# Optimization experiments

Measured on AMD Instinct MI355X. Metric: run time of the kernel, lower is better.

Reference implementation:

```python
import jax, jax.numpy as jnp
import numpy as np

N = 50000
E = 800000
T = 5            # towers
F = 10           # in_num / F_in per tower (divide_input=False)
F_OUT = 2        # out_channels // towers
G = 64           # number of graphs in the batch
L = 2            # conv layers
BN_EPS = 1e-5
STD_EPS = 1e-5


def setup_inputs() -> dict:
    key = jax.random.key(0)
    ks = jax.random.split(key, 24)
    s = 0.1
    inp = {
        'x': jax.random.normal(ks[0], (N, F), jnp.float32),
        'edge_emb': jax.random.normal(ks[1], (4, F), jnp.float32) * s,
        'mlp1_w1': jax.random.normal(ks[2], (F, 5), jnp.float32) * s,
        'mlp1_b1': jnp.zeros((5,), jnp.float32),
        'mlp1_w2': jax.random.normal(ks[3], (5, F), jnp.float32) * s,
        'mlp1_b2': jnp.zeros((F,), jnp.float32),
        'enc_w': jax.random.normal(ks[4], (L, F, F), jnp.float32) * s,
        'enc_b': jnp.zeros((L, F), jnp.float32),
        'pre_w': jax.random.normal(ks[5], (L, T, 3 * F, F), jnp.float32) * s,
        'pre_b': jnp.zeros((L, T, F), jnp.float32),
        'post_w': jax.random.normal(ks[6], (L, T, 13 * F, F_OUT), jnp.float32) * s,
        'post_b': jnp.zeros((L, T, F_OUT), jnp.float32),
        'lin_w': jax.random.normal(ks[7], (L, F, F), jnp.float32) * s,
        'lin_b': jnp.zeros((L, F), jnp.float32),
        'bn_gamma': jnp.ones((L, F), jnp.float32),
        'bn_beta': jnp.zeros((L, F), jnp.float32),
        'mlp2_w1': jax.random.normal(ks[8], (F, 5), jnp.float32) * s,
        'mlp2_b1': jnp.zeros((5,), jnp.float32),
        'mlp2_w2': jax.random.normal(ks[9], (5, 1), jnp.float32) * s,
        'mlp2_b2': jnp.zeros((1,), jnp.float32),
        'edge_index': jax.random.randint(ks[10], (2, E), 0, N, jnp.int64),
        'edge_attr': jax.random.randint(ks[11], (E,), 0, 4, jnp.int64),
        'batch': jnp.sort(jax.random.randint(ks[12], (N,), 0, G, jnp.int64)),
    }
    return inp


def reference(x, edge_emb, mlp1_w1, mlp1_b1, mlp1_w2, mlp1_b2,
              enc_w, enc_b, pre_w, pre_b, post_w, post_b, lin_w, lin_b,
              bn_gamma, bn_beta, mlp2_w1, mlp2_b1, mlp2_w2, mlp2_b2,
              edge_index, edge_attr, batch):
    src, dst = edge_index[0], edge_index[1]
    # mlp1: 10 -> 5 -> 10
    h = jax.nn.relu(x @ mlp1_w1 + mlp1_b1) @ mlp1_w2 + mlp1_b2  # [N, F]
    ea = edge_emb[edge_attr]  # [E, F] edge embedding lookup

    # in-degree at target nodes, PNA degree statistics
    deg = jax.ops.segment_sum(jnp.ones((src.shape[0],), h.dtype), dst, num_segments=N)
    d = jnp.clip(deg, 1.0)
    avg_log = jnp.mean(jnp.log(deg + 1.0))  # avg_deg['log'] from degree distribution
    log_d = jnp.log(d + 1.0)
    amp = (log_d / avg_log)[:, None, None]
    att = (avg_log / log_d)[:, None, None]
    has_in = (deg > 0)[:, None, None]
    inv_d = (1.0 / d)[:, None, None]

    for l in range(L):
        e = ea @ enc_w[l] + enc_b[l]  # [E, F]
        # message = pre_nn(cat(x_i, x_j, edge_attr)) per tower (x shared across towers)
        msg_in = jnp.concatenate([h[dst], h[src], e], axis=-1)  # [E, 3F]
        m = jnp.einsum('ef,tfo->eto', msg_in, pre_w[l]) + pre_b[l]  # [E, T, F]
        mean = jax.ops.segment_sum(m, dst, num_segments=N) * inv_d
        mean2 = jax.ops.segment_sum(m * m, dst, num_segments=N) * inv_d
        std = jnp.sqrt(jax.nn.relu(mean2 - mean * mean) + STD_EPS)
        mn = jnp.where(has_in, jax.ops.segment_min(m, dst, num_segments=N), 0.0)
        mx = jnp.where(has_in, jax.ops.segment_max(m, dst, num_segments=N), 0.0)
        agg = jnp.concatenate([mean, mn, mx, std], axis=-1)  # [N, T, 4F]
        agg = jnp.concatenate([agg, agg * amp, agg * att], axis=-1)  # [N, T, 12F]
        xt = jnp.broadcast_to(h[:, None, :], (h.shape[0], T, F))
        o = jnp.concatenate([xt, agg], axis=-1)  # [N, T, 13F]
        o = jnp.einsum('ntf,tfo->nto', o, post_w[l]) + post_b[l]  # [N, T, F_OUT]
        o = o.reshape(o.shape[0], T * F_OUT) @ lin_w[l] + lin_b[l]  # [N, F]
        # train-mode BatchNorm over nodes
        mu = jnp.mean(o, axis=0)
        var = jnp.var(o, axis=0)
        o = (o - mu) / jnp.sqrt(var + BN_EPS) * bn_gamma[l] + bn_beta[l]
        h = jax.nn.relu(o)

    g = jax.ops.segment_sum(h, batch, num_segments=G)  # global_add_pool -> [G, F]
    out = jax.nn.relu(g @ mlp2_w1 + mlp2_b1) @ mlp2_w2 + mlp2_b2  # [G, 1]
    return out
```

## Files before the change

### kernel.cpp

```cpp
#include <hip/hip_runtime.h>
#include <math.h>

#define N_NODES 50000
#define N_EDGES 800000
#define G_GRAPHS 64
#define BSTRIDE 64
#define CPAD 16

#define WAVE_SYNC() asm volatile("s_waitcnt lgkmcnt(0)" ::: "memory")
#define RFL(v) __builtin_amdgcn_readfirstlane(v)

__global__ void k_mlp1(const float* __restrict__ x,
                       const float* __restrict__ w1, const float* __restrict__ b1,
                       const float* __restrict__ w2, const float* __restrict__ b2,
                       float* __restrict__ h,
                       int* __restrict__ cnt,
                       float* __restrict__ bn_part, float* __restrict__ g,
                       float* __restrict__ avg_log,
                       const float* __restrict__ edge_emb,
                       const float* __restrict__ enc_w, const float* __restrict__ enc_b,
                       const float* __restrict__ pre_w, float* __restrict__ encm,
                       float* __restrict__ u) {
  __shared__ float eo[2][4][10];
  __shared__ float sw[500];
  int tid = threadIdx.x;
  int n = blockIdx.x * blockDim.x + tid;
  if (n < 1280) bn_part[n] = 0.f;
  if (n < G_GRAPHS * 10) g[n] = 0.f;
  if (n == 0) avg_log[0] = 0.f;

  bool act = n < N_NODES;
  float hr[10];
  if (act) {
    cnt[n * CPAD] = 0;
    float xv[10];
#pragma unroll
    for (int k = 0; k < 10; k++) xv[k] = x[n * 10 + k];
    float hid[5];
#pragma unroll
    for (int j = 0; j < 5; j++) {
      float a = b1[j];
#pragma unroll
      for (int k = 0; k < 10; k++) a += xv[k] * w1[k * 5 + j];
      hid[j] = fmaxf(a, 0.f);
    }
#pragma unroll
    for (int f = 0; f < 10; f++) {
      float a = b2[f];
#pragma unroll
      for (int j = 0; j < 5; j++) a += hid[j] * w2[j * 10 + f];
      hr[f] = a;
      h[n * 10 + f] = a;
    }
  }
  for (int j = tid; j < 500; j += 256) {
    int t = j / 100, k = (j / 10) % 10, f = j % 10;
    sw[j] = pre_w[(t * 30 + 10 + k) * 10 + f];
  }
  if (blockIdx.x == 0) {
    for (int i = tid; i < 80; i += 256) {
      int l = i / 40; int a = (i / 10) % 4; int k = i % 10;
      float s = enc_b[l * 10 + k];
      for (int j = 0; j < 10; j++) s += edge_emb[a * 10 + j] * enc_w[(l * 10 + j) * 10 + k];
      eo[l][a][k] = s;
    }
  }
  __syncthreads();
  if (blockIdx.x == 0) {
    for (int i = tid; i < 400; i += 256) {
      int l = i / 200; int a = (i / 50) % 4; int t = (i / 10) % 5; int f = i % 10;
      float s = 0.f;
      for (int k = 0; k < 10; k++) s += eo[l][a][k] * pre_w[((l * 5 + t) * 30 + 20 + k) * 10 + f];
      encm[i] = s;
    }
  }
  if (act) {
    float2* up = (float2*)(u + n * 50);
#pragma unroll
    for (int c0 = 0; c0 < 25; c0++) {
      int ca = 2 * c0, cb = 2 * c0 + 1;
      int ta = ca / 10, fa = ca % 10, tb = cb / 10, fb = cb % 10;
      float a = 0.f, b = 0.f;
#pragma unroll
      for (int k = 0; k < 10; k++) {
        a += hr[k] * sw[ta * 100 + fa + k * 10];
        b += hr[k] * sw[tb * 100 + fb + k * 10];
      }
      up[c0] = make_float2(a, b);
    }
  }
}

__global__ void k_scatter(const int* __restrict__ src, const int* __restrict__ dst,
                          const int* __restrict__ attr,
                          int* __restrict__ cnt, int* __restrict__ epk) {
  int e = blockIdx.x * blockDim.x + threadIdx.x;
  if (e >= N_EDGES) return;
  int d = dst[e];
  int s = src[e];
  int a = attr[e];
  int k = atomicAdd(&cnt[d * CPAD], 1);
  if (k < BSTRIDE) epk[d * BSTRIDE + k] = s * 200 + a;
}

__global__ void k_avg(const int* __restrict__ cnt, float* __restrict__ avg_log) {
  __shared__ float ws[4];
  int tid = threadIdx.x;
  float acc = 0.f;
  for (int n = blockIdx.x * 256 + tid; n < N_NODES; n += gridDim.x * 256)
    acc += __logf((float)cnt[n * CPAD] + 1.f);
#pragma unroll
  for (int d = 32; d >= 1; d >>= 1) acc += __shfl_down(acc, d, 64);
  if ((tid & 63) == 0) ws[tid >> 6] = acc;
  __syncthreads();
  if (tid == 0) atomicAdd(avg_log, ws[0] + ws[1] + ws[2] + ws[3]);
}

__global__ __launch_bounds__(256) void k_conv(
    const float* __restrict__ h,
    const float* __restrict__ u,
    const float* __restrict__ pre_w_l,
    const float* __restrict__ pre_b_l,
    const float* __restrict__ post_w_l,
    const float* __restrict__ post_b_l,
    const float* __restrict__ lin_w_l,
    const float* __restrict__ lin_b_l,
    const float* __restrict__ encm_l,
    const int* __restrict__ cnt,
    const int* __restrict__ epk,
    const float* __restrict__ avg_log_p,
    float* __restrict__ o_buf,
    float* __restrict__ bn_part)
{
  __shared__ float sW[1300];
  __shared__ float sLin[100];
  __shared__ float sLb[10];
  __shared__ float sPb[10];
  __shared__ float sP[4][100];
  __shared__ float sO[4][10];
  __shared__ float bnS[10], bnQ[10];

  int tid = threadIdx.x;
  int wid = RFL(tid >> 6);
  int lane = tid & 63;
  for (int i = tid; i < 1300; i += 256) sW[i] = post_w_l[i];
  for (int i = tid; i < 100; i += 256) sLin[i] = lin_w_l[i];
  if (tid < 10) {
    sLb[tid] = lin_b_l[tid];
    sPb[tid] = post_b_l[tid];
    bnS[tid] = 0.f; bnQ[tid] = 0.f;
  }
  __syncthreads();

  int f = lane % 10;
  int t = (lane < 50) ? (lane / 10) : 4;
  int c50 = t * 10 + f;
  const char* ub = (const char*)u;
  int c50_4 = c50 * 4;
  float wdst[10];
#pragma unroll
  for (int k = 0; k < 10; k++) wdst[k] = pre_w_l[(t * 30 + k) * 10 + f];
  float em0 = encm_l[c50];
  float em1 = encm_l[50 + c50];
  float em2 = encm_l[100 + c50];
  float em3 = encm_l[150 + c50];
  float preb = pre_b_l[c50];
  float avg_log = avg_log_p[0] * (1.f / N_NODES);

  int n = blockIdx.x * 4 + wid;
  float bnSv = 0.f, bnQv = 0.f;

#define PRE(US, AS, IDX) { int sp_ = __builtin_amdgcn_readlane(pk, (IDX) & 63); \
    AS = sp_ & 3; US = 0.f; \
    if ((IDX) < deg) US = *(const float*)(ub + (sp_ & ~7) + c50_4); }
#define PROC(US, AS) { float m_ = ((AS & 2) ? ((AS & 1) ? bem3 : bem2) : ((AS & 1) ? bem1 : bem0)) + US; \
    sum += m_; sq = fmaf(m_, m_, sq); mnv = fminf(mnv, m_); mxv = fmaxf(mxv, m_); }

  if (n < N_NODES) {
    int deg = cnt[n * CPAD];
    if (deg > BSTRIDE) deg = BSTRIDE;
    int pk = (lane < deg) ? epk[n * BSTRIDE + lane] : 0;

    const float* hn = h + n * 10;
    float2 d0 = *(const float2*)hn;
    float2 d1 = *(const float2*)(hn + 2);
    float2 d2 = *(const float2*)(hn + 4);
    float2 d3 = *(const float2*)(hn + 6);
    float2 d4 = *(const float2*)(hn + 8);
    float xf = hn[f];

    float base = preb
      + d0.x * wdst[0] + d0.y * wdst[1] + d1.x * wdst[2] + d1.y * wdst[3]
      + d2.x * wdst[4] + d2.y * wdst[5] + d3.x * wdst[6] + d3.y * wdst[7]
      + d4.x * wdst[8] + d4.y * wdst[9];
    float bem0 = base + em0, bem1 = base + em1, bem2 = base + em2, bem3 = base + em3;

    float sum = 0.f, sq = 0.f, mnv = INFINITY, mxv = -INFINITY;
    {
      float u0, u1, u2, u3, u4, u5, u6, u7;
      int a0, a1, a2, a3, a4, a5, a6, a7;
      PRE(u0, a0, 0) PRE(u1, a1, 1) PRE(u2, a2, 2) PRE(u3, a3, 3)
      PRE(u4, a4, 4) PRE(u5, a5, 5) PRE(u6, a6, 6) PRE(u7, a7, 7)
      int full = deg & ~7;
      int jb = 0;
      for (; jb < full; jb += 8) {
        PROC(u0, a0) PRE(u0, a0, jb + 8)
        PROC(u1, a1) PRE(u1, a1, jb + 9)
        PROC(u2, a2) PRE(u2, a2, jb + 10)
        PROC(u3, a3) PRE(u3, a3, jb + 11)
        PROC(u4, a4) PRE(u4, a4, jb + 12)
        PROC(u5, a5) PRE(u5, a5, jb + 13)
        PROC(u6, a6) PRE(u6, a6, jb + 14)
        PROC(u7, a7) PRE(u7, a7, jb + 15)
      }
      if (jb + 0 < deg) PROC(u0, a0)
      if (jb + 1 < deg) PROC(u1, a1)
      if (jb + 2 < deg) PROC(u2, a2)
      if (jb + 3 < deg) PROC(u3, a3)
      if (jb + 4 < deg) PROC(u4, a4)
      if (jb + 5 < deg) PROC(u5, a5)
      if (jb + 6 < deg) PROC(u6, a6)
    }

    float degf = (float)deg;
    float d = fmaxf(degf, 1.f);
    float inv = 1.f / d;
    float mean = sum * inv;
    float var = sq * inv - mean * mean;
    float stdv = sqrtf(fmaxf(var, 0.f) + 1e-5f);
    if (deg == 0) { mnv = 0.f; mxv = 0.f; }
    float log_d = logf(d + 1.f);
    float amp = log_d / avg_log;
    float att = avg_log / log_d;

    float vv[13];
    vv[0] = xf;
    vv[1] = mean;       vv[2] = mnv;        vv[3] = mxv;        vv[4] = stdv;
    vv[5] = mean * amp; vv[6] = mnv * amp;  vv[7] = mxv * amp;  vv[8] = stdv * amp;
    vv[9] = mean * att; vv[10] = mnv * att; vv[11] = mxv * att; vv[12] = stdv * att;
    float p0 = 0.f, p1 = 0.f;
#pragma unroll
    for (int j = 0; j < 13; j++) {
      const float2 w = *(const float2*)&sW[t * 260 + (f + 10 * j) * 2];
      p0 += vv[j] * w.x; p1 += vv[j] * w.y;
    }
    if (lane < 50) *(float2*)&sP[wid][c50 * 2] = make_float2(p0, p1);
    WAVE_SYNC();
    if (lane < 10) {
      int tt = lane >> 1, c = lane & 1;
      float o = sPb[lane];
#pragma unroll
      for (int ff = 0; ff < 10; ff++) o += sP[wid][(tt * 10 + ff) * 2 + c];
      sO[wid][lane] = o;
    }
    WAVE_SYNC();
    if (lane < 10) {
      float r = sLb[lane];
#pragma unroll
      for (int j = 0; j < 10; j++) r += sO[wid][j] * sLin[j * 10 + lane];
      o_buf[n * 10 + lane] = r;
      bnSv = r; bnQv = r * r;
    }
  }
#undef PRE
#undef PROC

  if (lane < 10) {
    atomicAdd(&bnS[lane], bnSv);
    atomicAdd(&bnQ[lane], bnQv);
  }
  __syncthreads();
  if (tid < 20) {
    float v = (tid < 10) ? bnS[tid] : bnQ[tid - 10];
    atomicAdd(&bn_part[(blockIdx.x & 31) * 20 + tid], v);
  }
}

__global__ __launch_bounds__(256) void k_bnpool(
    const float* __restrict__ o_buf,
    const float* __restrict__ bn_part,
    const float* __restrict__ gamma, const float* __restrict__ beta,
    float* __restrict__ h,
    const int* __restrict__ batch, float* __restrict__ g,
    const float* __restrict__ pre_w_next, float* __restrict__ u,
    int do_u, int do_pool) {
  __shared__ float sS[20];
  __shared__ float sMu[10], sInv[10];
  __shared__ float pool[8][10];
  __shared__ float hrow[25][10];
  __shared__ float sw[500];
  __shared__ int g0s;
  int tid = threadIdx.x;
  int n0 = blockIdx.x * 25;
  if (do_u) {
    for (int j = tid; j < 500; j += 256) {
      int t = j / 100, k = (j / 10) % 10, f = j % 10;
      sw[j] = pre_w_next[(t * 30 + 10 + k) * 10 + f];
    }
  }
  if (tid < 20) {
    float s = 0.f;
    for (int j = 0; j < 32; j++) s += bn_part[j * 20 + tid];
    sS[tid] = s;
  }
  if (tid < 80) pool[tid / 10][tid % 10] = 0.f;
  if (tid == 0) g0s = batch[n0];
  __syncthreads();
  if (tid < 10) {
    float mu = sS[tid] * (1.f / N_NODES);
    float var = sS[10 + tid] * (1.f / N_NODES) - mu * mu;
    sMu[tid] = mu;
    sInv[tid] = 1.f / sqrtf(fmaxf(var, 0.f) + 1e-5f);
  }
  __syncthreads();
  if (tid < 250) {
    int dn = tid / 10, f = tid % 10;
    int n = n0 + dn;
    int i = n * 10 + f;
    float o = (o_buf[i] - sMu[f]) * sInv[f] * gamma[f] + beta[f];
    float r = fmaxf(o, 0.f);
    h[i] = r;
    hrow[dn][f] = r;
    if (do_pool) {
      int dg = batch[n] - g0s;
      if (dg < 8) atomicAdd(&pool[dg][f], r);
      else atomicAdd(&g[(g0s + dg) * 10 + f], r);
    }
  }
  __syncthreads();
  if (do_u && tid < 250) {
#pragma unroll
    for (int it = 0; it < 5; it++) {
      int j = tid + it * 250;
      int node = j / 50, c = j % 50;
      int t = c / 10, f2 = c % 10;
      float acc = 0.f;
#pragma unroll
      for (int k = 0; k < 10; k++) acc += hrow[node][k] * sw[t * 100 + f2 + k * 10];
      u[n0 * 50 + j] = acc;
    }
  }
  if (do_pool) {
    __syncthreads();
    if (tid < 80) {
      float v = pool[tid / 10][tid % 10];
      if (v != 0.f) atomicAdd(&g[(g0s + tid / 10) * 10 + tid % 10], v);
    }
  }
}

__global__ void k_mlp2(const float* __restrict__ g,
                       const float* __restrict__ w1, const float* __restrict__ b1,
                       const float* __restrict__ w2, const float* __restrict__ b2,
                       float* __restrict__ out) {
  int b = threadIdx.x;
  if (b >= G_GRAPHS) return;
  float gv[10];
#pragma unroll
  for (int k = 0; k < 10; k++) gv[k] = g[b * 10 + k];
  float acc = b2[0];
#pragma unroll
  for (int j = 0; j < 5; j++) {
    float a = b1[j];
#pragma unroll
    for (int k = 0; k < 10; k++) a += gv[k] * w1[k * 5 + j];
    acc += fmaxf(a, 0.f) * w2[j];
  }
  out[b] = acc;
}

extern "C" void kernel_launch(void* const* d_in, const int* in_sizes, int n_in,
                              void* d_out, int out_size, void* d_ws, size_t ws_size,
                              hipStream_t stream) {
  const float* x        = (const float*)d_in[0];
  const float* edge_emb = (const float*)d_in[1];
  const float* m1w1 = (const float*)d_in[2];
  const float* m1b1 = (const float*)d_in[3];
  const float* m1w2 = (const float*)d_in[4];
  const float* m1b2 = (const float*)d_in[5];
  const float* enc_w = (const float*)d_in[6];
  const float* enc_b = (const float*)d_in[7];
  const float* pre_w = (const float*)d_in[8];
  const float* pre_b = (const float*)d_in[9];
  const float* post_w = (const float*)d_in[10];
  const float* post_b = (const float*)d_in[11];
  const float* lin_w = (const float*)d_in[12];
  const float* lin_b = (const float*)d_in[13];
  const float* bn_g = (const float*)d_in[14];
  const float* bn_b = (const float*)d_in[15];
  const float* m2w1 = (const float*)d_in[16];
  const float* m2b1 = (const float*)d_in[17];
  const float* m2w2 = (const float*)d_in[18];
  const float* m2b2 = (const float*)d_in[19];
  const int* edge_index = (const int*)d_in[20];
  const int* edge_attr  = (const int*)d_in[21];
  const int* batch      = (const int*)d_in[22];
  const int* src  = edge_index;
  const int* dstp = edge_index + N_EDGES;

  char* ws = (char*)d_ws;
  size_t off = 0;
  auto alloc = [&](size_t bytes) {
    void* p = ws + off;
    off += (bytes + 255) & ~(size_t)255;
    return p;
  };
  float*     h       = (float*)alloc(N_NODES * 10 * sizeof(float));
  float*     o_buf   = (float*)alloc(N_NODES * 10 * sizeof(float));
  float*     u       = (float*)alloc((size_t)(N_NODES * 50 + 64) * sizeof(float));
  int*       cnt     = (int*)alloc((size_t)N_NODES * CPAD * sizeof(int));
  int*       epk     = (int*)alloc((size_t)N_NODES * BSTRIDE * sizeof(int));
  float*     encm    = (float*)alloc(400 * sizeof(float));
  float*     avg_log = (float*)alloc(16);
  float*     bn_part = (float*)alloc(2 * 32 * 20 * sizeof(float));
  float*     g       = (float*)alloc(G_GRAPHS * 10 * sizeof(float));

  k_mlp1<<<(N_NODES + 255) / 256, 256, 0, stream>>>(x, m1w1, m1b1, m1w2, m1b2, h,
                                                    cnt, bn_part, g, avg_log,
                                                    edge_emb, enc_w, enc_b, pre_w, encm, u);
  k_scatter<<<(N_EDGES + 255) / 256, 256, 0, stream>>>(src, dstp, edge_attr, cnt, epk);
  k_avg<<<64, 256, 0, stream>>>(cnt, avg_log);

  for (int l = 0; l < 2; l++) {
    k_conv<<<(N_NODES + 3) / 4, 256, 0, stream>>>(
        h, u, pre_w + l * 1500, pre_b + l * 50, post_w + l * 1300, post_b + l * 10,
        lin_w + l * 100, lin_b + l * 10, encm + l * 200,
        cnt, epk, avg_log, o_buf, bn_part + l * 640);
    k_bnpool<<<N_NODES / 25, 256, 0, stream>>>(
        o_buf, bn_part + l * 640, bn_g + l * 10, bn_b + l * 10, h, batch, g,
        pre_w + 1500, u, l == 0, l == 1);
  }
  k_mlp2<<<1, 64, 0, stream>>>(g, m2w1, m2b1, m2w2, m2b2, (float*)d_out);
}
```

Measured before the change: 293.1 us.

## Drop precomputed u projection; gather raw h and project per edge in conv

Removes the per-node precomputed source projection buffer u (50 floats per node) and instead gathers the 10-float h row of each source node, applying the pre-transform weights per edge with cross-lane readlane dot products. It also fuses the mlp1 and edge-scatter kernels into one edge-sized front kernel with a separate counter-zero kernel, and pads the edge lists with sentinel entries pointing to a zeroed h row so the gather needs no bounds check. This cuts gather traffic and removes the u writes in mlp1 and bnpool, at the cost of about 10 extra readlane+FMA steps per edge in the conv kernel.

Result: slower. 348.7 us (+19.0%).

```diff
diff --git a/kernel.cpp b/kernel.cpp
--- a/kernel.cpp
+++ b/kernel.cpp
@@ -6,36 +6,49 @@
 #define G_GRAPHS 64
 #define BSTRIDE 64
 #define CPAD 16
+#define SENPK (N_NODES * 40)
 
 #define WAVE_SYNC() asm volatile("s_waitcnt lgkmcnt(0)" ::: "memory")
 #define RFL(v) __builtin_amdgcn_readfirstlane(v)
-
-__global__ void k_mlp1(const float* __restrict__ x,
-                       const float* __restrict__ w1, const float* __restrict__ b1,
-                       const float* __restrict__ w2, const float* __restrict__ b2,
-                       float* __restrict__ h,
-                       int* __restrict__ cnt,
-                       float* __restrict__ bn_part, float* __restrict__ g,
-                       float* __restrict__ avg_log,
-                       const float* __restrict__ edge_emb,
-                       const float* __restrict__ enc_w, const float* __restrict__ enc_b,
-                       const float* __restrict__ pre_w, float* __restrict__ encm,
-                       float* __restrict__ u) {
+#define RLF(v, k) __int_as_float(__builtin_amdgcn_readlane(__float_as_int(v), (k)))
+
+__global__ void k_zero(int* __restrict__ cnt) {
+  int n = blockIdx.x * 256 + threadIdx.x;
+  if (n < N_NODES) cnt[n * CPAD] = 0;
+}
+
+__global__ __launch_bounds__(256) void k_front(
+    const float* __restrict__ x,
+    const float* __restrict__ w1, const float* __restrict__ b1,
+    const float* __restrict__ w2, const float* __restrict__ b2,
+    float* __restrict__ h,
+    int* __restrict__ cnt,
+    float* __restrict__ bn_part, float* __restrict__ g,
+    float* __restrict__ avg_log,
+    const float* __restrict__ edge_emb,
+    const float* __restrict__ enc_w, const float* __restrict__ enc_b,
+    const float* __restrict__ pre_w, float* __restrict__ encm,
+    const int* __restrict__ src, const int* __restrict__ dst,
+    const int* __restrict__ attr, int* __restrict__ epk) {
   __shared__ float eo[2][4][10];
-  __shared__ float sw[500];
   int tid = threadIdx.x;
-  int n = blockIdx.x * blockDim.x + tid;
-  if (n < 1280) bn_part[n] = 0.f;
-  if (n < G_GRAPHS * 10) g[n] = 0.f;
-  if (n == 0) avg_log[0] = 0.f;
-
-  bool act = n < N_NODES;
-  float hr[10];
-  if (act) {
-    cnt[n * CPAD] = 0;
+  int gid = blockIdx.x * 256 + tid;
+
+  int ed = dst[gid];
+  int es = src[gid];
+  int ea = attr[gid];
+  int rk = atomicAdd(&cnt[ed * CPAD], 1);
+
+  if (gid < 1280) bn_part[gid] = 0.f;
+  if (gid < G_GRAPHS * 10) g[gid] = 0.f;
+  if (gid == 0) avg_log[0] = 0.f;
+  { int z = gid - N_NODES; if (z >= 0 && z < 16) h[N_NODES * 10 + z] = 0.f; }
+
+  if (gid < N_NODES) {
+    const float2* xp = (const float2*)(x + gid * 10);
     float xv[10];
 #pragma unroll
-    for (int k = 0; k < 10; k++) xv[k] = x[n * 10 + k];
+    for (int k = 0; k < 5; k++) { float2 v = xp[k]; xv[2 * k] = v.x; xv[2 * k + 1] = v.y; }
     float hid[5];
 #pragma unroll
     for (int j = 0; j < 5; j++) {
@@ -49,14 +62,12 @@
       float a = b2[f];
 #pragma unroll
       for (int j = 0; j < 5; j++) a += hid[j] * w2[j * 10 + f];
-      hr[f] = a;
-      h[n * 10 + f] = a;
-    }
-  }
-  for (int j = tid; j < 500; j += 256) {
-    int t = j / 100, k = (j / 10) % 10, f = j % 10;
-    sw[j] = pre_w[(t * 30 + 10 + k) * 10 + f];
-  }
+      h[gid * 10 + f] = a;
+    }
+  }
+
+  if (rk < BSTRIDE) epk[ed * BSTRIDE + rk] = es * 40 + ea;
+
   if (blockIdx.x == 0) {
     for (int i = tid; i < 80; i += 256) {
       int l = i / 40; int a = (i / 10) % 4; int k = i % 10;
@@ -74,41 +85,20 @@
       encm[i] = s;
     }
   }
-  if (act) {
-    float2* up = (float2*)(u + n * 50);
-#pragma unroll
-    for (int c0 = 0; c0 < 25; c0++) {
-      int ca = 2 * c0, cb = 2 * c0 + 1;
-      int ta = ca / 10, fa = ca % 10, tb = cb / 10, fb = cb % 10;
-      float a = 0.f, b = 0.f;
-#pragma unroll
-      for (int k = 0; k < 10; k++) {
-        a += hr[k] * sw[ta * 100 + fa + k * 10];
-        b += hr[k] * sw[tb * 100 + fb + k * 10];
-      }
-      up[c0] = make_float2(a, b);
-    }
-  }
-}
-
-__global__ void k_scatter(const int* __restrict__ src, const int* __restrict__ dst,
-                          const int* __restrict__ attr,
-                          int* __restrict__ cnt, int* __restrict__ epk) {
-  int e = blockIdx.x * blockDim.x + threadIdx.x;
-  if (e >= N_EDGES) return;
-  int d = dst[e];
-  int s = src[e];
-  int a = attr[e];
-  int k = atomicAdd(&cnt[d * CPAD], 1);
-  if (k < BSTRIDE) epk[d * BSTRIDE + k] = s * 200 + a;
-}
-
-__global__ void k_avg(const int* __restrict__ cnt, float* __restrict__ avg_log) {
+}
+
+__global__ void k_avg(const int* __restrict__ cnt, float* __restrict__ avg_log,
+                      int* __restrict__ epk) {
   __shared__ float ws[4];
   int tid = threadIdx.x;
   float acc = 0.f;
-  for (int n = blockIdx.x * 256 + tid; n < N_NODES; n += gridDim.x * 256)
-    acc += __logf((float)cnt[n * CPAD] + 1.f);
+  for (int n = blockIdx.x * 256 + tid; n < N_NODES; n += gridDim.x * 256) {
+    int dg = cnt[n * CPAD];
+    acc += __logf((float)dg + 1.f);
+    int dd = dg < BSTRIDE ? dg : BSTRIDE;
+    int end = dd + 8 < BSTRIDE ? dd + 8 : BSTRIDE;
+    for (int j = dd; j < end; j++) epk[n * BSTRIDE + j] = SENPK;
+  }
 #pragma unroll
   for (int d = 32; d >= 1; d >>= 1) acc += __shfl_down(acc, d, 64);
   if ((tid & 63) == 0) ws[tid >> 6] = acc;
@@ -118,7 +108,6 @@
 
 __global__ __launch_bounds__(256) void k_conv(
     const float* __restrict__ h,
-    const float* __restrict__ u,
     const float* __restrict__ pre_w_l,
     const float* __restrict__ pre_b_l,
     const float* __restrict__ post_w_l,
@@ -155,11 +144,13 @@
   int f = lane % 10;
   int t = (lane < 50) ? (lane / 10) : 4;
   int c50 = t * 10 + f;
-  const char* ub = (const char*)u;
-  int c50_4 = c50 * 4;
-  float wdst[10];
+  const char* hb = (const char*)h;
+  int f4 = f * 4;
+  float wdst[10], wsrc[10];
 #pragma unroll
   for (int k = 0; k < 10; k++) wdst[k] = pre_w_l[(t * 30 + k) * 10 + f];
+#pragma unroll
+  for (int k = 0; k < 10; k++) wsrc[k] = pre_w_l[(t * 30 + 10 + k) * 10 + f];
   float em0 = encm_l[c50];
   float em1 = encm_l[50 + c50];
   float em2 = encm_l[100 + c50];
@@ -170,16 +161,19 @@
   int n = blockIdx.x * 4 + wid;
   float bnSv = 0.f, bnQv = 0.f;
 
-#define PRE(US, AS, IDX) { int sp_ = __builtin_amdgcn_readlane(pk, (IDX) & 63); \
-    AS = sp_ & 3; US = 0.f; \
-    if ((IDX) < deg) US = *(const float*)(ub + (sp_ & ~7) + c50_4); }
-#define PROC(US, AS) { float m_ = ((AS & 2) ? ((AS & 1) ? bem3 : bem2) : ((AS & 1) ? bem1 : bem0)) + US; \
+#define PRE(HV, AS, IDX) { int sp_ = __builtin_amdgcn_readlane(pk, (IDX) & 63); \
+    AS = sp_ & 3; \
+    HV = *(const float*)(hb + (sp_ & ~7) + f4); }
+#define PROC(HV, AS) { float us_ = 0.f; \
+    _Pragma("unroll") \
+    for (int k_ = 0; k_ < 10; k_++) us_ += RLF(HV, k_) * wsrc[k_]; \
+    float m_ = ((AS & 2) ? ((AS & 1) ? bem3 : bem2) : ((AS & 1) ? bem1 : bem0)) + us_; \
     sum += m_; sq = fmaf(m_, m_, sq); mnv = fminf(mnv, m_); mxv = fmaxf(mxv, m_); }
 
   if (n < N_NODES) {
-    int deg = cnt[n * CPAD];
+    int deg = RFL(cnt[n * CPAD]);
     if (deg > BSTRIDE) deg = BSTRIDE;
-    int pk = (lane < deg) ? epk[n * BSTRIDE + lane] : 0;
+    int pk = epk[n * BSTRIDE + lane];
 
     const float* hn = h + n * 10;
     float2 d0 = *(const float2*)hn;
@@ -282,22 +276,13 @@
     const float* __restrict__ gamma, const float* __restrict__ beta,
     float* __restrict__ h,
     const int* __restrict__ batch, float* __restrict__ g,
-    const float* __restrict__ pre_w_next, float* __restrict__ u,
-    int do_u, int do_pool) {
+    int do_pool) {
   __shared__ float sS[20];
   __shared__ float sMu[10], sInv[10];
   __shared__ float pool[8][10];
-  __shared__ float hrow[25][10];
-  __shared__ float sw[500];
   __shared__ int g0s;
   int tid = threadIdx.x;
   int n0 = blockIdx.x * 25;
-  if (do_u) {
-    for (int j = tid; j < 500; j += 256) {
-      int t = j / 100, k = (j / 10) % 10, f = j % 10;
-      sw[j] = pre_w_next[(t * 30 + 10 + k) * 10 + f];
-    }
-  }
   if (tid < 20) {
     float s = 0.f;
     for (int j = 0; j < 32; j++) s += bn_part[j * 20 + tid];
@@ -320,24 +305,10 @@
     float o = (o_buf[i] - sMu[f]) * sInv[f] * gamma[f] + beta[f];
     float r = fmaxf(o, 0.f);
     h[i] = r;
-    hrow[dn][f] = r;
     if (do_pool) {
       int dg = batch[n] - g0s;
       if (dg < 8) atomicAdd(&pool[dg][f], r);
       else atomicAdd(&g[(g0s + dg) * 10 + f], r);
-    }
-  }
-  __syncthreads();
-  if (do_u && tid < 250) {
-#pragma unroll
-    for (int it = 0; it < 5; it++) {
-      int j = tid + it * 250;
-      int node = j / 50, c = j % 50;
-      int t = c / 10, f2 = c % 10;
-      float acc = 0.f;
-#pragma unroll
-      for (int k = 0; k < 10; k++) acc += hrow[node][k] * sw[t * 100 + f2 + k * 10];
-      u[n0 * 50 + j] = acc;
     }
   }
   if (do_pool) {
@@ -405,9 +376,8 @@
     off += (bytes + 255) & ~(size_t)255;
     return p;
   };
-  float*     h       = (float*)alloc(N_NODES * 10 * sizeof(float));
+  float*     h       = (float*)alloc((N_NODES * 10 + 16) * sizeof(float));
   float*     o_buf   = (float*)alloc(N_NODES * 10 * sizeof(float));
-  float*     u       = (float*)alloc((size_t)(N_NODES * 50 + 64) * sizeof(float));
   int*       cnt     = (int*)alloc((size_t)N_NODES * CPAD * sizeof(int));
   int*       epk     = (int*)alloc((size_t)N_NODES * BSTRIDE * sizeof(int));
   float*     encm    = (float*)alloc(400 * sizeof(float));
@@ -415,20 +385,22 @@
   float*     bn_part = (float*)alloc(2 * 32 * 20 * sizeof(float));
   float*     g       = (float*)alloc(G_GRAPHS * 10 * sizeof(float));
 
-  k_mlp1<<<(N_NODES + 255) / 256, 256, 0, stream>>>(x, m1w1, m1b1, m1w2, m1b2, h,
-                                                    cnt, bn_part, g, avg_log,
-                                                    edge_emb, enc_w, enc_b, pre_w, encm, u);
-  k_scatter<<<(N_EDGES + 255) / 256, 256, 0, stream>>>(src, dstp, edge_attr, cnt, epk);
-  k_avg<<<64, 256, 0, stream>>>(cnt, avg_log);
+  k_zero<<<(N_NODES + 255) / 256, 256, 0, stream>>>(cnt);
+
+  k_front<<<N_EDGES / 256, 256, 0, stream>>>(x, m1w1, m1b1, m1w2, m1b2, h,
+                                             cnt, bn_part, g, avg_log,
+                                             edge_emb, enc_w, enc_b, pre_w, encm,
+                                             src, dstp, edge_attr, epk);
+  k_avg<<<64, 256, 0, stream>>>(cnt, avg_log, epk);
 
   for (int l = 0; l < 2; l++) {
-    k_conv<<<(N_NODES + 3) / 4, 256, 0, stream>>>(
-        h, u, pre_w + l * 1500, pre_b + l * 50, post_w + l * 1300, post_b + l * 10,
+    k_conv<<<N_NODES / 4, 256, 0, stream>>>(
+        h, pre_w + l * 1500, pre_b + l * 50, post_w + l * 1300, post_b + l * 10,
         lin_w + l * 100, lin_b + l * 10, encm + l * 200,
         cnt, epk, avg_log, o_buf, bn_part + l * 640);
     k_bnpool<<<N_NODES / 25, 256, 0, stream>>>(
         o_buf, bn_part + l * 640, bn_g + l * 10, bn_b + l * 10, h, batch, g,
-        pre_w + 1500, u, l == 0, l == 1);
+        l == 1);
   }
   k_mlp2<<<1, 64, 0, stream>>>(g, m2w1, m2b1, m2w2, m2b2, (float*)d_out);
 }
```

## Fuse edge scatter into front kernel and process two nodes per wave in conv

Applied to the files above, without the earlier changes.

Merges the mlp1/precompute kernel with the edge-bucketing scatter into one edge-sized launch, adding a small zeroing kernel for the counters beforehand. The average-degree kernel now fills eight padding slots past each node's degree with a sentinel that points at a zeroed tail of u, so the conv loop can drop its per-edge bounds check. The conv kernel now gives each wave two nodes and interleaves their gather loops to keep more loads in flight and halve the grid. The trade-offs are higher register pressure, a serialized post-processing loop with extra wave syncs, and an extra launch.

Result: faster. 270.1 us (-7.8%).

```diff
diff --git a/kernel.cpp b/kernel.cpp
--- a/kernel.cpp
+++ b/kernel.cpp
@@ -6,36 +6,52 @@
 #define G_GRAPHS 64
 #define BSTRIDE 64
 #define CPAD 16
+#define SENPK (N_NODES * 200)
 
 #define WAVE_SYNC() asm volatile("s_waitcnt lgkmcnt(0)" ::: "memory")
 #define RFL(v) __builtin_amdgcn_readfirstlane(v)
 
-__global__ void k_mlp1(const float* __restrict__ x,
-                       const float* __restrict__ w1, const float* __restrict__ b1,
-                       const float* __restrict__ w2, const float* __restrict__ b2,
-                       float* __restrict__ h,
-                       int* __restrict__ cnt,
-                       float* __restrict__ bn_part, float* __restrict__ g,
-                       float* __restrict__ avg_log,
-                       const float* __restrict__ edge_emb,
-                       const float* __restrict__ enc_w, const float* __restrict__ enc_b,
-                       const float* __restrict__ pre_w, float* __restrict__ encm,
-                       float* __restrict__ u) {
+__global__ void k_zero(int* __restrict__ cnt) {
+  int n = blockIdx.x * 256 + threadIdx.x;
+  if (n < N_NODES) cnt[n * CPAD] = 0;
+}
+
+__global__ __launch_bounds__(256) void k_front(
+    const float* __restrict__ x,
+    const float* __restrict__ w1, const float* __restrict__ b1,
+    const float* __restrict__ w2, const float* __restrict__ b2,
+    float* __restrict__ h,
+    int* __restrict__ cnt,
+    float* __restrict__ bn_part, float* __restrict__ g,
+    float* __restrict__ avg_log,
+    const float* __restrict__ edge_emb,
+    const float* __restrict__ enc_w, const float* __restrict__ enc_b,
+    const float* __restrict__ pre_w, float* __restrict__ encm,
+    float* __restrict__ u,
+    const int* __restrict__ src, const int* __restrict__ dst,
+    const int* __restrict__ attr, int* __restrict__ epk) {
   __shared__ float eo[2][4][10];
   __shared__ float sw[500];
   int tid = threadIdx.x;
-  int n = blockIdx.x * blockDim.x + tid;
-  if (n < 1280) bn_part[n] = 0.f;
-  if (n < G_GRAPHS * 10) g[n] = 0.f;
-  if (n == 0) avg_log[0] = 0.f;
-
-  bool act = n < N_NODES;
+  int gid = blockIdx.x * 256 + tid;
+
+  int ed = dst[gid];
+  int es = src[gid];
+  int ea = attr[gid];
+  int rk = atomicAdd(&cnt[ed * CPAD], 1);
+
+  if (gid < 1280) bn_part[gid] = 0.f;
+  if (gid < G_GRAPHS * 10) g[gid] = 0.f;
+  if (gid == 0) avg_log[0] = 0.f;
+  { int z = gid - N_NODES; if (z >= 0 && z < 64) u[N_NODES * 50 + z] = 0.f; }
+
+  bool act = gid < N_NODES;
   float hr[10];
   if (act) {
-    cnt[n * CPAD] = 0;
+    const float2* xp = (const float2*)(x + gid * 10);
     float xv[10];
 #pragma unroll
-    for (int k = 0; k < 10; k++) xv[k] = x[n * 10 + k];
+    for (int k = 0; k < 5; k++) { float2 v = xp[k]; xv[2 * k] = v.x; xv[2 * k + 1] = v.y; }
     float hid[5];
 #pragma unroll
     for (int j = 0; j < 5; j++) {
@@ -50,13 +66,17 @@
 #pragma unroll
       for (int j = 0; j < 5; j++) a += hid[j] * w2[j * 10 + f];
       hr[f] = a;
-      h[n * 10 + f] = a;
-    }
-  }
+      h[gid * 10 + f] = a;
+    }
+  }
+
   for (int j = tid; j < 500; j += 256) {
     int t = j / 100, k = (j / 10) % 10, f = j % 10;
     sw[j] = pre_w[(t * 30 + 10 + k) * 10 + f];
   }
+
+  if (rk < BSTRIDE) epk[ed * BSTRIDE + rk] = es * 200 + ea;
+
   if (blockIdx.x == 0) {
     for (int i = tid; i < 80; i += 256) {
       int l = i / 40; int a = (i / 10) % 4; int k = i % 10;
@@ -74,8 +94,9 @@
       encm[i] = s;
     }
   }
+
   if (act) {
-    float2* up = (float2*)(u + n * 50);
+    float2* up = (float2*)(u + gid * 50);
 #pragma unroll
     for (int c0 = 0; c0 < 25; c0++) {
       int ca = 2 * c0, cb = 2 * c0 + 1;
@@ -91,24 +112,18 @@
   }
 }
 
-__global__ void k_scatter(const int* __restrict__ src, const int* __restrict__ dst,
-                          const int* __restrict__ attr,
-                          int* __restrict__ cnt, int* __restrict__ epk) {
-  int e = blockIdx.x * blockDim.x + threadIdx.x;
-  if (e >= N_EDGES) return;
-  int d = dst[e];
-  int s = src[e];
-  int a = attr[e];
-  int k = atomicAdd(&cnt[d * CPAD], 1);
-  if (k < BSTRIDE) epk[d * BSTRIDE + k] = s * 200 + a;
-}
-
-__global__ void k_avg(const int* __restrict__ cnt, float* __restrict__ avg_log) {
+__global__ void k_avg(const int* __restrict__ cnt, float* __restrict__ avg_log,
+                      int* __restrict__ epk) {
   __shared__ float ws[4];
   int tid = threadIdx.x;
   float acc = 0.f;
-  for (int n = blockIdx.x * 256 + tid; n < N_NODES; n += gridDim.x * 256)
-    acc += __logf((float)cnt[n * CPAD] + 1.f);
+  for (int n = blockIdx.x * 256 + tid; n < N_NODES; n += gridDim.x * 256) {
+    int dg = cnt[n * CPAD];
+    acc += __logf((float)dg + 1.f);
+    int dd = dg < BSTRIDE ? dg : BSTRIDE;
+    int end = dd + 8 < BSTRIDE ? dd + 8 : BSTRIDE;
+    for (int j = dd; j < end; j++) epk[n * BSTRIDE + j] = SENPK;
+  }
 #pragma unroll
   for (int d = 32; d >= 1; d >>= 1) acc += __shfl_down(acc, d, 64);
   if ((tid & 63) == 0) ws[tid >> 6] = acc;
@@ -167,60 +182,102 @@
   float preb = pre_b_l[c50];
   float avg_log = avg_log_p[0] * (1.f / N_NODES);
 
-  int n = blockIdx.x * 4 + wid;
+  int nA = (blockIdx.x * 4 + wid) * 2;
+  int nB = nA + 1;
   float bnSv = 0.f, bnQv = 0.f;
 
-#define PRE(US, AS, IDX) { int sp_ = __builtin_amdgcn_readlane(pk, (IDX) & 63); \
-    AS = sp_ & 3; US = 0.f; \
-    if ((IDX) < deg) US = *(const float*)(ub + (sp_ & ~7) + c50_4); }
-#define PROC(US, AS) { float m_ = ((AS & 2) ? ((AS & 1) ? bem3 : bem2) : ((AS & 1) ? bem1 : bem0)) + US; \
-    sum += m_; sq = fmaf(m_, m_, sq); mnv = fminf(mnv, m_); mxv = fmaxf(mxv, m_); }
-
-  if (n < N_NODES) {
-    int deg = cnt[n * CPAD];
-    if (deg > BSTRIDE) deg = BSTRIDE;
-    int pk = (lane < deg) ? epk[n * BSTRIDE + lane] : 0;
-
-    const float* hn = h + n * 10;
-    float2 d0 = *(const float2*)hn;
-    float2 d1 = *(const float2*)(hn + 2);
-    float2 d2 = *(const float2*)(hn + 4);
-    float2 d3 = *(const float2*)(hn + 6);
-    float2 d4 = *(const float2*)(hn + 8);
-    float xf = hn[f];
-
-    float base = preb
-      + d0.x * wdst[0] + d0.y * wdst[1] + d1.x * wdst[2] + d1.y * wdst[3]
-      + d2.x * wdst[4] + d2.y * wdst[5] + d3.x * wdst[6] + d3.y * wdst[7]
-      + d4.x * wdst[8] + d4.y * wdst[9];
-    float bem0 = base + em0, bem1 = base + em1, bem2 = base + em2, bem3 = base + em3;
-
-    float sum = 0.f, sq = 0.f, mnv = INFINITY, mxv = -INFINITY;
-    {
-      float u0, u1, u2, u3, u4, u5, u6, u7;
-      int a0, a1, a2, a3, a4, a5, a6, a7;
-      PRE(u0, a0, 0) PRE(u1, a1, 1) PRE(u2, a2, 2) PRE(u3, a3, 3)
-      PRE(u4, a4, 4) PRE(u5, a5, 5) PRE(u6, a6, 6) PRE(u7, a7, 7)
-      int full = deg & ~7;
-      int jb = 0;
-      for (; jb < full; jb += 8) {
-        PROC(u0, a0) PRE(u0, a0, jb + 8)
-        PROC(u1, a1) PRE(u1, a1, jb + 9)
-        PROC(u2, a2) PRE(u2, a2, jb + 10)
-        PROC(u3, a3) PRE(u3, a3, jb + 11)
-        PROC(u4, a4) PRE(u4, a4, jb + 12)
-        PROC(u5, a5) PRE(u5, a5, jb + 13)
-        PROC(u6, a6) PRE(u6, a6, jb + 14)
-        PROC(u7, a7) PRE(u7, a7, jb + 15)
-      }
-      if (jb + 0 < deg) PROC(u0, a0)
-      if (jb + 1 < deg) PROC(u1, a1)
-      if (jb + 2 < deg) PROC(u2, a2)
-      if (jb + 3 < deg) PROC(u3, a3)
-      if (jb + 4 < deg) PROC(u4, a4)
-      if (jb + 5 < deg) PROC(u5, a5)
-      if (jb + 6 < deg) PROC(u6, a6)
-    }
+  int degA = RFL(cnt[nA * CPAD]);
+  int degB = RFL(cnt[nB * CPAD]);
+  if (degA > BSTRIDE) degA = BSTRIDE;
+  if (degB > BSTRIDE) degB = BSTRIDE;
+  int pkA = epk[nA * BSTRIDE + lane];
+  int pkB = epk[nB * BSTRIDE + lane];
+
+  const float* hnA = h + nA * 10;
+  const float* hnB = h + nB * 10;
+  float2 a0_ = *(const float2*)hnA, a1_ = *(const float2*)(hnA + 2),
+         a2_ = *(const float2*)(hnA + 4), a3_ = *(const float2*)(hnA + 6),
+         a4_ = *(const float2*)(hnA + 8);
+  float2 b0_ = *(const float2*)hnB, b1_ = *(const float2*)(hnB + 2),
+         b2_ = *(const float2*)(hnB + 4), b3_ = *(const float2*)(hnB + 6),
+         b4_ = *(const float2*)(hnB + 8);
+  float xfA = hnA[f], xfB = hnB[f];
+
+  float baseA = preb
+    + a0_.x * wdst[0] + a0_.y * wdst[1] + a1_.x * wdst[2] + a1_.y * wdst[3]
+    + a2_.x * wdst[4] + a2_.y * wdst[5] + a3_.x * wdst[6] + a3_.y * wdst[7]
+    + a4_.x * wdst[8] + a4_.y * wdst[9];
+  float baseB = preb
+    + b0_.x * wdst[0] + b0_.y * wdst[1] + b1_.x * wdst[2] + b1_.y * wdst[3]
+    + b2_.x * wdst[4] + b2_.y * wdst[5] + b3_.x * wdst[6] + b3_.y * wdst[7]
+    + b4_.x * wdst[8] + b4_.y * wdst[9];
+  float bemA0 = baseA + em0, bemA1 = baseA + em1, bemA2 = baseA + em2, bemA3 = baseA + em3;
+  float bemB0 = baseB + em0, bemB1 = baseB + em1, bemB2 = baseB + em2, bemB3 = baseB + em3;
+
+  float sumA = 0.f, sqA = 0.f, mnA = INFINITY, mxA = -INFINITY;
+  float sumB = 0.f, sqB = 0.f, mnB = INFINITY, mxB = -INFINITY;
+
+#define PREA(S, IDX) { int sp_ = __builtin_amdgcn_readlane(pkA, (IDX) & 63); \
+    aA##S = sp_ & 3; uA##S = *(const float*)(ub + (sp_ & ~7) + c50_4); }
+#define PREB(S, IDX) { int sp_ = __builtin_amdgcn_readlane(pkB, (IDX) & 63); \
+    aB##S = sp_ & 3; uB##S = *(const float*)(ub + (sp_ & ~7) + c50_4); }
+#define PROCA(S) { float m_ = ((aA##S & 2) ? ((aA##S & 1) ? bemA3 : bemA2) : ((aA##S & 1) ? bemA1 : bemA0)) + uA##S; \
+    sumA += m_; sqA = fmaf(m_, m_, sqA); mnA = fminf(mnA, m_); mxA = fmaxf(mxA, m_); }
+#define PROCB(S) { float m_ = ((aB##S & 2) ? ((aB##S & 1) ? bemB3 : bemB2) : ((aB##S & 1) ? bemB1 : bemB0)) + uB##S; \
+    sumB += m_; sqB = fmaf(m_, m_, sqB); mnB = fminf(mnB, m_); mxB = fmaxf(mxB, m_); }
+
+  {
+    float uA0, uA1, uA2, uA3, uB0, uB1, uB2, uB3;
+    int aA0, aA1, aA2, aA3, aB0, aB1, aB2, aB3;
+    PREA(0, 0) PREB(0, 0) PREA(1, 1) PREB(1, 1)
+    PREA(2, 2) PREB(2, 2) PREA(3, 3) PREB(3, 3)
+    int jmA = degA & ~3, jmB = degB & ~3;
+    int mm = jmA < jmB ? jmA : jmB;
+    int j = 0;
+    for (; j < mm; j += 4) {
+      PROCA(0) PREA(0, j + 4)
+      PROCB(0) PREB(0, j + 4)
+      PROCA(1) PREA(1, j + 5)
+      PROCB(1) PREB(1, j + 5)
+      PROCA(2) PREA(2, j + 6)
+      PROCB(2) PREB(2, j + 6)
+      PROCA(3) PREA(3, j + 7)
+      PROCB(3) PREB(3, j + 7)
+    }
+    int jA = j, jB = j;
+    for (; jA < jmA; jA += 4) {
+      PROCA(0) PREA(0, jA + 4)
+      PROCA(1) PREA(1, jA + 5)
+      PROCA(2) PREA(2, jA + 6)
+      PROCA(3) PREA(3, jA + 7)
+    }
+    for (; jB < jmB; jB += 4) {
+      PROCB(0) PREB(0, jB + 4)
+      PROCB(1) PREB(1, jB + 5)
+      PROCB(2) PREB(2, jB + 6)
+      PROCB(3) PREB(3, jB + 7)
+    }
+    if (jA + 0 < degA) PROCA(0)
+    if (jA + 1 < degA) PROCA(1)
+    if (jA + 2 < degA) PROCA(2)
+    if (jB + 0 < degB) PROCB(0)
+    if (jB + 1 < degB) PROCB(1)
+    if (jB + 2 < degB) PROCB(2)
+  }
+#undef PREA
+#undef PREB
+#undef PROCA
+#undef PROCB
+
+#pragma unroll
+  for (int sel = 0; sel < 2; sel++) {
+    int n = sel ? nB : nA;
+    int deg = sel ? degB : degA;
+    float sum = sel ? sumB : sumA;
+    float sq = sel ? sqB : sqA;
+    float mnv = sel ? mnB : mnA;
+    float mxv = sel ? mxB : mxA;
+    float xf = sel ? xfB : xfA;
 
     float degf = (float)deg;
     float d = fmaxf(degf, 1.f);
@@ -259,11 +316,10 @@
 #pragma unroll
       for (int j = 0; j < 10; j++) r += sO[wid][j] * sLin[j * 10 + lane];
       o_buf[n * 10 + lane] = r;
-      bnSv = r; bnQv = r * r;
-    }
-  }
-#undef PRE
-#undef PROC
+      bnSv += r; bnQv += r * r;
+    }
+    WAVE_SYNC();
+  }
 
   if (lane < 10) {
     atomicAdd(&bnS[lane], bnSv);
@@ -415,14 +471,16 @@
   float*     bn_part = (float*)alloc(2 * 32 * 20 * sizeof(float));
   float*     g       = (float*)alloc(G_GRAPHS * 10 * sizeof(float));
 
-  k_mlp1<<<(N_NODES + 255) / 256, 256, 0, stream>>>(x, m1w1, m1b1, m1w2, m1b2, h,
-                                                    cnt, bn_part, g, avg_log,
-                                                    edge_emb, enc_w, enc_b, pre_w, encm, u);
-  k_scatter<<<(N_EDGES + 255) / 256, 256, 0, stream>>>(src, dstp, edge_attr, cnt, epk);
-  k_avg<<<64, 256, 0, stream>>>(cnt, avg_log);
+  k_zero<<<(N_NODES + 255) / 256, 256, 0, stream>>>(cnt);
+
+  k_front<<<N_EDGES / 256, 256, 0, stream>>>(x, m1w1, m1b1, m1w2, m1b2, h,
+                                             cnt, bn_part, g, avg_log,
+                                             edge_emb, enc_w, enc_b, pre_w, encm, u,
+                                             src, dstp, edge_attr, epk);
+  k_avg<<<64, 256, 0, stream>>>(cnt, avg_log, epk);
 
   for (int l = 0; l < 2; l++) {
-    k_conv<<<(N_NODES + 3) / 4, 256, 0, stream>>>(
+    k_conv<<<N_NODES / 8, 256, 0, stream>>>(
         h, u, pre_w + l * 1500, pre_b + l * 50, post_w + l * 1300, post_b + l * 10,
         lin_w + l * 100, lin_b + l * 10, encm + l * 200,
         cnt, epk, avg_log, o_buf, bn_part + l * 640);
```
